# Optimization experiments

Hardware: AMD Instinct MI355X
Metric: run time of the kernel (lower is better)

Reference implementation:

```python
import jax, jax.numpy as jnp
import numpy as np

B, N, D, T = 64, 512, 128, 8  # batch, atoms, atom_embedding_dim, num_bond_types
NEG_SLOPE = 0.2


def setup_inputs() -> dict:
    key = jax.random.key(0)
    k1, k2, k3, k4 = jax.random.split(key, 4)
    src = jax.random.normal(k1, (B, N, D), dtype=jnp.float32)
    dst = jax.random.normal(k2, (B, N, D), dtype=jnp.float32)
    # bond-type index per (i,j) pair; -1 means 'no bond' (masked)
    edges = jax.random.randint(k3, (B, N, N), -1, T, dtype=jnp.int32)
    # xavier_uniform with gain=1.414 on shape (2*D*T, 1)
    fan_in, fan_out = 2 * D * T, 1
    bound = 1.414 * np.sqrt(6.0 / (fan_in + fan_out))
    a = jax.random.uniform(k4, (2 * D * T, 1), minval=-bound, maxval=bound,
                           dtype=jnp.float32)
    return {"src_embeddings": src, "dst_embeddings": dst, "edges": edges, "a": a}


def reference(src_embeddings, dst_embeddings, edges, a):
    b, n, d = src_embeddings.shape
    t = a.shape[0] // (2 * d)
    # a row-block k (length 2d) is the weight for bond type k:
    # score = a_k[:d] . src_i + a_k[d:] . dst_j
    a_mat = a.reshape(t, 2 * d)
    a_src, a_dst = a_mat[:, :d], a_mat[:, d:]
    s_src = jnp.einsum('bnd,td->bnt', src_embeddings, a_src)  # (B,N,T)
    s_dst = jnp.einsum('bnd,td->bnt', dst_embeddings, a_dst)  # (B,N,T)
    k = jnp.clip(edges, 0, t - 1)                             # (B,N,N)
    bi = jnp.arange(b)[:, None, None]
    gi = jnp.arange(n)[None, :, None]
    gj = jnp.arange(n)[None, None, :]
    g = s_src[bi, gi, k] + s_dst[bi, gj, k]                   # (B,N,N)
    scores = jnp.where(edges >= 0, g, jnp.zeros((), g.dtype))
    return jnp.where(scores >= 0, scores, NEG_SLOPE * scores)
```

## Files before the change

kernel.cpp:

```cpp
#include <hip/hip_runtime.h>

#define BB 64
#define NN 512
#define DD 128
#define TT 8
#define NEG_SLOPE 0.2f

typedef float f32x4 __attribute__((ext_vector_type(4)));
typedef int i32x4 __attribute__((ext_vector_type(4)));

__global__ __launch_bounds__(256) void precompute_scores(
    const float* __restrict__ src, const float* __restrict__ dst,
    const float* __restrict__ a, float* __restrict__ s_src,
    float* __restrict__ s_dstT) {
  const int tid = threadIdx.x;
  const int wave = tid >> 6;
  const int lane = tid & 63;
  const int sub = lane >> 4;
  const int sl = lane & 15;
  const int dd0 = sl * 8;

#pragma unroll
  for (int half = 0; half < 2; ++half) {
    const float* __restrict__ X = half ? dst : src;
    float ar[TT][8];
#pragma unroll
    for (int t = 0; t < TT; ++t) {
      const f32x4 a0 = *(const f32x4*)(a + t * 2 * DD + half * DD + dd0);
      const f32x4 a1 = *(const f32x4*)(a + t * 2 * DD + half * DD + dd0 + 4);
      ar[t][0] = a0.x; ar[t][1] = a0.y; ar[t][2] = a0.z; ar[t][3] = a0.w;
      ar[t][4] = a1.x; ar[t][5] = a1.y; ar[t][6] = a1.z; ar[t][7] = a1.w;
    }
#pragma unroll
    for (int pass = 0; pass < 2; ++pass) {
      const int r = pass * 16384 + blockIdx.x * 16 + wave * 4 + sub;
      const f32x4 x0 = *(const f32x4*)(X + (long)r * DD + dd0);
      const f32x4 x1 = *(const f32x4*)(X + (long)r * DD + dd0 + 4);

      float p[TT];
#pragma unroll
      for (int t = 0; t < TT; ++t) {
        p[t] = x0.x * ar[t][0] + x0.y * ar[t][1] + x0.z * ar[t][2] +
               x0.w * ar[t][3] + x1.x * ar[t][4] + x1.y * ar[t][5] +
               x1.z * ar[t][6] + x1.w * ar[t][7];
      }
#pragma unroll
      for (int t = 0; t < TT; ++t) {
        p[t] += __shfl_xor(p[t], 1, 64);
        p[t] += __shfl_xor(p[t], 2, 64);
        p[t] += __shfl_xor(p[t], 4, 64);
      }
      const int tk = sl & 7;
      float v = p[0];
      v = tk == 1 ? p[1] : v;
      v = tk == 2 ? p[2] : v;
      v = tk == 3 ? p[3] : v;
      v = tk == 4 ? p[4] : v;
      v = tk == 5 ? p[5] : v;
      v = tk == 6 ? p[6] : v;
      v = tk == 7 ? p[7] : v;
      v += __shfl_xor(v, 8, 64);

      if (sl < 8) {
        if (half == 0) {
          s_src[(long)r * TT + sl] = v;
        } else {
          const int b = r >> 9, n = r & 511;
          s_dstT[(long)b * NN * TT + sl * NN + n] = v;
        }
      }
    }
  }
}

__global__ __launch_bounds__(256) void edge_attention(
    const int* __restrict__ edges, const float* __restrict__ s_src,
    const float* __restrict__ s_dstT, float* __restrict__ out) {
  __shared__ float sdt[TT * NN];
  __shared__ float ssc[32 * TT];

  const int tid = threadIdx.x;
  const int b = blockIdx.x >> 4;
  const int i0 = (blockIdx.x & 15) * 32;

  const f32x4* __restrict__ g_sdt = (const f32x4*)(s_dstT + (long)b * NN * TT);
  f32x4* __restrict__ l_sdt = (f32x4*)sdt;
#pragma unroll
  for (int q = 0; q < 4; ++q) l_sdt[q * 256 + tid] = g_sdt[q * 256 + tid];

  if (tid < 64) {
    ((f32x4*)ssc)[tid] =
        ((const f32x4*)(s_src + ((long)b * NN + i0) * TT))[tid];
  }
  __syncthreads();

  const int rsub = tid >> 7;
  const int j0 = (tid & 127) * 4;

#pragma unroll 4
  for (int it = 0; it < 16; ++it) {
    const int r = it * 2 + rsub;
    const long base = ((long)(b * NN + i0 + r)) * NN + j0;
    const i32x4 e4 = *(const i32x4*)(edges + base);
    const float* __restrict__ sr = ssc + r * TT;

    const int ee[4] = {e4.x, e4.y, e4.z, e4.w};
    float oo[4];
#pragma unroll
    for (int m = 0; m < 4; ++m) {
      const int e = ee[m];
      const int k = e < 0 ? 0 : e;
      const float g = sr[k] + sdt[k * NN + j0 + m];
      const float v = e < 0 ? 0.0f : g;
      oo[m] = v >= 0.0f ? v : NEG_SLOPE * v;
    }
    const f32x4 o = {oo[0], oo[1], oo[2], oo[3]};
    __builtin_nontemporal_store(o, (f32x4*)(out + base));
  }
}

extern "C" void kernel_launch(void* const* d_in, const int* in_sizes, int n_in,
                              void* d_out, int out_size, void* d_ws, size_t ws_size,
                              hipStream_t stream) {
  const float* src = (const float*)d_in[0];
  const float* dst = (const float*)d_in[1];
  const int* edges = (const int*)d_in[2];
  const float* a = (const float*)d_in[3];
  float* out = (float*)d_out;

  float* s_src = (float*)d_ws;
  float* s_dstT = s_src + (long)BB * NN * TT;

  precompute_scores<<<1024, 256, 0, stream>>>(src, dst, a, s_src, s_dstT);

  edge_attention<<<BB * 16, 256, 0, stream>>>(edges, s_src, s_dstT, out);
}
```

Before: 155.6 us.

## Restructure score precompute and use padded j-major LDS layout with 512-thread blocks

The precompute kernel now gives each lane one bond type and a 16-element slice of D. It computes src and dst dots together over 8 rows and reduces them with cross-lane shuffles, replacing the earlier per-type select chain. The edge kernel stores destination scores in shared memory as j-major with a stride of 9 floats, so the gathered reads for different bond types fall in different LDS banks. The edge kernel also moves to 512-thread blocks with half the iterations per thread. The new shared-memory fill reads global memory with a transpose, which is less vectorized.

```diff
diff --git a/kernel.cpp b/kernel.cpp
--- a/kernel.cpp
+++ b/kernel.cpp
@@ -14,79 +14,65 @@
     const float* __restrict__ a, float* __restrict__ s_src,
     float* __restrict__ s_dstT) {
   const int tid = threadIdx.x;
-  const int wave = tid >> 6;
-  const int lane = tid & 63;
-  const int sub = lane >> 4;
-  const int sl = lane & 15;
-  const int dd0 = sl * 8;
+  const int wave = tid >> 6, lane = tid & 63;
+  const int t = lane & 7, dc = lane >> 3;
+  const int d0 = dc * 16;
+  const int r0 = (blockIdx.x * 4 + wave) * 8;
 
+  f32x4 as[4], ad[4];
 #pragma unroll
-  for (int half = 0; half < 2; ++half) {
-    const float* __restrict__ X = half ? dst : src;
-    float ar[TT][8];
+  for (int i = 0; i < 4; ++i) {
+    as[i] = *(const f32x4*)(a + t * 2 * DD + d0 + 4 * i);
+    ad[i] = *(const f32x4*)(a + t * 2 * DD + DD + d0 + 4 * i);
+  }
+
+  float ps[8], pd[8];
 #pragma unroll
-    for (int t = 0; t < TT; ++t) {
-      const f32x4 a0 = *(const f32x4*)(a + t * 2 * DD + half * DD + dd0);
-      const f32x4 a1 = *(const f32x4*)(a + t * 2 * DD + half * DD + dd0 + 4);
-      ar[t][0] = a0.x; ar[t][1] = a0.y; ar[t][2] = a0.z; ar[t][3] = a0.w;
-      ar[t][4] = a1.x; ar[t][5] = a1.y; ar[t][6] = a1.z; ar[t][7] = a1.w;
+  for (int ri = 0; ri < 8; ++ri) {
+    const long r = r0 + ri;
+    float p = 0.f, q = 0.f;
+#pragma unroll
+    for (int i = 0; i < 4; ++i) {
+      const f32x4 x = *(const f32x4*)(src + r * DD + d0 + 4 * i);
+      p += x.x * as[i].x + x.y * as[i].y + x.z * as[i].z + x.w * as[i].w;
+      const f32x4 y = *(const f32x4*)(dst + r * DD + d0 + 4 * i);
+      q += y.x * ad[i].x + y.y * ad[i].y + y.z * ad[i].z + y.w * ad[i].w;
     }
+    p += __shfl_xor(p, 8, 64);
+    p += __shfl_xor(p, 16, 64);
+    p += __shfl_xor(p, 32, 64);
+    q += __shfl_xor(q, 8, 64);
+    q += __shfl_xor(q, 16, 64);
+    q += __shfl_xor(q, 32, 64);
+    ps[ri] = p;
+    pd[ri] = q;
+  }
+
+  float vs = ps[0], vd = pd[0];
 #pragma unroll
-    for (int pass = 0; pass < 2; ++pass) {
-      const int r = pass * 16384 + blockIdx.x * 16 + wave * 4 + sub;
-      const f32x4 x0 = *(const f32x4*)(X + (long)r * DD + dd0);
-      const f32x4 x1 = *(const f32x4*)(X + (long)r * DD + dd0 + 4);
-
-      float p[TT];
-#pragma unroll
-      for (int t = 0; t < TT; ++t) {
-        p[t] = x0.x * ar[t][0] + x0.y * ar[t][1] + x0.z * ar[t][2] +
-               x0.w * ar[t][3] + x1.x * ar[t][4] + x1.y * ar[t][5] +
-               x1.z * ar[t][6] + x1.w * ar[t][7];
-      }
-#pragma unroll
-      for (int t = 0; t < TT; ++t) {
-        p[t] += __shfl_xor(p[t], 1, 64);
-        p[t] += __shfl_xor(p[t], 2, 64);
-        p[t] += __shfl_xor(p[t], 4, 64);
-      }
-      const int tk = sl & 7;
-      float v = p[0];
-      v = tk == 1 ? p[1] : v;
-      v = tk == 2 ? p[2] : v;
-      v = tk == 3 ? p[3] : v;
-      v = tk == 4 ? p[4] : v;
-      v = tk == 5 ? p[5] : v;
-      v = tk == 6 ? p[6] : v;
-      v = tk == 7 ? p[7] : v;
-      v += __shfl_xor(v, 8, 64);
-
-      if (sl < 8) {
-        if (half == 0) {
-          s_src[(long)r * TT + sl] = v;
-        } else {
-          const int b = r >> 9, n = r & 511;
-          s_dstT[(long)b * NN * TT + sl * NN + n] = v;
-        }
-      }
-    }
+  for (int ri = 1; ri < 8; ++ri) {
+    vs = dc == ri ? ps[ri] : vs;
+    vd = dc == ri ? pd[ri] : vd;
   }
+  const int rr = r0 + dc;
+  s_src[(long)rr * TT + t] = vs;
+  const int b = rr >> 9, n = rr & 511;
+  s_dstT[((long)b * TT + t) * NN + n] = vd;
 }
 
-__global__ __launch_bounds__(256) void edge_attention(
+__global__ __launch_bounds__(512) void edge_attention(
     const int* __restrict__ edges, const float* __restrict__ s_src,
     const float* __restrict__ s_dstT, float* __restrict__ out) {
-  __shared__ float sdt[TT * NN];
+  __shared__ float sdt[NN * 9];
   __shared__ float ssc[32 * TT];
 
   const int tid = threadIdx.x;
   const int b = blockIdx.x >> 4;
   const int i0 = (blockIdx.x & 15) * 32;
 
-  const f32x4* __restrict__ g_sdt = (const f32x4*)(s_dstT + (long)b * NN * TT);
-  f32x4* __restrict__ l_sdt = (f32x4*)sdt;
+  const float* __restrict__ g_sdt = s_dstT + (long)b * NN * TT;
 #pragma unroll
-  for (int q = 0; q < 4; ++q) l_sdt[q * 256 + tid] = g_sdt[q * 256 + tid];
+  for (int q = 0; q < TT; ++q) sdt[tid * 9 + q] = g_sdt[q * NN + tid];
 
   if (tid < 64) {
     ((f32x4*)ssc)[tid] =
@@ -98,8 +84,8 @@
   const int j0 = (tid & 127) * 4;
 
 #pragma unroll 4
-  for (int it = 0; it < 16; ++it) {
-    const int r = it * 2 + rsub;
+  for (int it = 0; it < 8; ++it) {
+    const int r = it * 4 + rsub;
     const long base = ((long)(b * NN + i0 + r)) * NN + j0;
     const i32x4 e4 = *(const i32x4*)(edges + base);
     const float* __restrict__ sr = ssc + r * TT;
@@ -110,7 +96,7 @@
     for (int m = 0; m < 4; ++m) {
       const int e = ee[m];
       const int k = e < 0 ? 0 : e;
-      const float g = sr[k] + sdt[k * NN + j0 + m];
+      const float g = sr[k] + sdt[(j0 + m) * 9 + k];
       const float v = e < 0 ? 0.0f : g;
       oo[m] = v >= 0.0f ? v : NEG_SLOPE * v;
     }
@@ -133,5 +119,5 @@
 
   precompute_scores<<<1024, 256, 0, stream>>>(src, dst, a, s_src, s_dstT);
 
-  edge_attention<<<BB * 16, 256, 0, stream>>>(edges, s_src, s_dstT, out);
+  edge_attention<<<BB * 16, 512, 0, stream>>>(edges, s_src, s_dstT, out);
 }
```

Measured after the change: 165.6 us. 1.06x slower.

## Hold dst scores in registers with select tree and smaller edge tiles

Applied to the files above, without the earlier changes.

The edge kernel no longer stages the per-batch dst score table in LDS. Each thread loads its 8 bond-type dst scores for its 4 columns into registers and picks the right one with a 3-level select tree. Tiles shrink to 16 rows by 256 columns, giving 4x more blocks, and all edge loads are issued before the barrier to overlap memory latency. The output store drops the nontemporal hint, and the relu-like step becomes fmaxf. This removes LDS gather traffic and bank conflicts but adds register pressure and redundant global reads of s_dstT across blocks.

```diff
diff --git a/kernel.cpp b/kernel.cpp
--- a/kernel.cpp
+++ b/kernel.cpp
@@ -66,7 +66,7 @@
           s_src[(long)r * TT + sl] = v;
         } else {
           const int b = r >> 9, n = r & 511;
-          s_dstT[(long)b * NN * TT + sl * NN + n] = v;
+          s_dstT[((long)b * TT + sl) * NN + n] = v;
         }
       }
     }
@@ -76,46 +76,58 @@
 __global__ __launch_bounds__(256) void edge_attention(
     const int* __restrict__ edges, const float* __restrict__ s_src,
     const float* __restrict__ s_dstT, float* __restrict__ out) {
-  __shared__ float sdt[TT * NN];
-  __shared__ float ssc[32 * TT];
+  __shared__ float ssc[16 * TT];
 
   const int tid = threadIdx.x;
-  const int b = blockIdx.x >> 4;
-  const int i0 = (blockIdx.x & 15) * 32;
+  const int wave = tid >> 6, lane = tid & 63;
+  const int bid = blockIdx.x;
+  const int jhalf = bid & 1;
+  const int itile = (bid >> 1) & 31;
+  const int b = bid >> 6;
+  const int i0 = itile * 16;
+  const int j0 = jhalf * 256 + lane * 4;
 
-  const f32x4* __restrict__ g_sdt = (const f32x4*)(s_dstT + (long)b * NN * TT);
-  f32x4* __restrict__ l_sdt = (f32x4*)sdt;
+  const float* __restrict__ sdb = s_dstT + (long)b * NN * TT;
+  f32x4 sd[TT];
 #pragma unroll
-  for (int q = 0; q < 4; ++q) l_sdt[q * 256 + tid] = g_sdt[q * 256 + tid];
+  for (int t = 0; t < TT; ++t) sd[t] = *(const f32x4*)(sdb + t * NN + j0);
 
-  if (tid < 64) {
+  i32x4 e4[4];
+#pragma unroll
+  for (int it = 0; it < 4; ++it) {
+    const long rbase = ((long)(b * NN + i0 + it * 4 + wave)) * NN + j0;
+    e4[it] = *(const i32x4*)(edges + rbase);
+  }
+
+  if (tid < 32) {
     ((f32x4*)ssc)[tid] =
         ((const f32x4*)(s_src + ((long)b * NN + i0) * TT))[tid];
   }
   __syncthreads();
 
-  const int rsub = tid >> 7;
-  const int j0 = (tid & 127) * 4;
-
-#pragma unroll 4
-  for (int it = 0; it < 16; ++it) {
-    const int r = it * 2 + rsub;
-    const long base = ((long)(b * NN + i0 + r)) * NN + j0;
-    const i32x4 e4 = *(const i32x4*)(edges + base);
-    const float* __restrict__ sr = ssc + r * TT;
-
-    const int ee[4] = {e4.x, e4.y, e4.z, e4.w};
+#pragma unroll
+  for (int it = 0; it < 4; ++it) {
+    const int r = it * 4 + wave;
+    const long rbase = ((long)(b * NN + i0 + r)) * NN + j0;
+    const int es[4] = {e4[it].x, e4[it].y, e4[it].z, e4[it].w};
     float oo[4];
 #pragma unroll
     for (int m = 0; m < 4; ++m) {
-      const int e = ee[m];
+      const int e = es[m];
       const int k = e < 0 ? 0 : e;
-      const float g = sr[k] + sdt[k * NN + j0 + m];
-      const float v = e < 0 ? 0.0f : g;
-      oo[m] = v >= 0.0f ? v : NEG_SLOPE * v;
+      const float a0 = (k & 1) ? sd[1][m] : sd[0][m];
+      const float a1 = (k & 1) ? sd[3][m] : sd[2][m];
+      const float a2 = (k & 1) ? sd[5][m] : sd[4][m];
+      const float a3 = (k & 1) ? sd[7][m] : sd[6][m];
+      const float b0 = (k & 2) ? a1 : a0;
+      const float b1 = (k & 2) ? a3 : a2;
+      const float dsel = (k & 4) ? b1 : b0;
+      const float g = ssc[r * TT + k] + dsel;
+      const float w = fmaxf(g, NEG_SLOPE * g);
+      oo[m] = e < 0 ? 0.0f : w;
     }
     const f32x4 o = {oo[0], oo[1], oo[2], oo[3]};
-    __builtin_nontemporal_store(o, (f32x4*)(out + base));
+    *(f32x4*)(out + rbase) = o;
   }
 }
 
@@ -133,5 +145,5 @@
 
   precompute_scores<<<1024, 256, 0, stream>>>(src, dst, a, s_src, s_dstT);
 
-  edge_attention<<<BB * 16, 256, 0, stream>>>(edges, s_src, s_dstT, out);
+  edge_attention<<<BB * 64, 256, 0, stream>>>(edges, s_src, s_dstT, out);
 }
```

New measurement: 148.7 us. 4.4% less time.
